# Kernel optimization log

Measured on AMD Instinct MI355X. Metric: run time of the kernel, lower is better.

Reference implementation:

```python
import jax, jax.numpy as jnp
import numpy as np

N = 50000      # nodes
E = 800000     # edges
F_IN = 128     # num_node_features
H = 128        # hidden_channels
C = 10         # num_classes
G = 512        # graphs in batch


def setup_inputs() -> dict:
    key = jax.random.key(0)
    ks = jax.random.split(key, 8)
    x = jax.random.normal(ks[0], (N, F_IN), dtype=jnp.float32)
    edge_index = jax.random.randint(ks[1], (2, E), 0, N, dtype=jnp.int64)
    batch = jnp.sort(jax.random.randint(ks[2], (N,), 0, G, dtype=jnp.int64))
    s = 1.0 / np.sqrt(F_IN)
    W1 = jax.random.normal(ks[3], (F_IN, H), dtype=jnp.float32) * s
    b1 = jnp.zeros((H,), dtype=jnp.float32)
    W2 = jax.random.normal(ks[4], (H, H), dtype=jnp.float32) * s
    b2 = jnp.zeros((H,), dtype=jnp.float32)
    Wl = jax.random.normal(ks[5], (H, C), dtype=jnp.float32) * s
    bl = jnp.zeros((C,), dtype=jnp.float32)
    return {"x": x, "edge_index": edge_index, "batch": batch,
            "W1": W1, "b1": b1, "W2": W2, "b2": b2, "Wl": Wl, "bl": bl}


def _gcn_conv(h, src, dst, deg_inv_sqrt, W, b):
    # PyG GCNConv: x @ W, then symmetric-normalized scatter-add with self-loops.
    h = h @ W                                   # [N, H]
    norm = deg_inv_sqrt[src] * deg_inv_sqrt[dst]  # [E]
    msg = h[src] * norm[:, None]                # gather + scale, [E, H]
    out = jax.ops.segment_sum(msg, dst, num_segments=N)
    # self-loop contribution (deg already includes +1):
    out = out + h * (deg_inv_sqrt * deg_inv_sqrt)[:, None]
    return out + b


def reference(x, edge_index, batch, W1, b1, W2, b2, Wl, bl):
    src, dst = edge_index[0], edge_index[1]
    # degree on destination nodes, +1 for self-loops (PyG default)
    deg = jax.ops.segment_sum(jnp.ones((E,), x.dtype), dst, num_segments=N) + 1.0
    deg_inv_sqrt = jax.lax.rsqrt(deg)

    h = jax.nn.relu(_gcn_conv(x, src, dst, deg_inv_sqrt, W1, b1))
    h = jax.nn.relu(_gcn_conv(h, src, dst, deg_inv_sqrt, W2, b2))

    # global mean pool over graphs
    sums = jax.ops.segment_sum(h, batch, num_segments=G)          # [G, H]
    counts = jax.ops.segment_sum(jnp.ones((N,), h.dtype), batch, num_segments=G)
    pooled = sums / jnp.clip(counts, 1.0)[:, None]
    # dropout p=0.5 is identity in eval mode
    return pooled @ Wl + bl
```

## Files before the change

kernel.cpp:

```cpp
#include <hip/hip_runtime.h>
#include <hip/hip_bf16.h>
#include <hip/hip_fp16.h>

typedef unsigned short ushort_t;
typedef unsigned int uint32;
typedef __attribute__((ext_vector_type(8))) short short8;
typedef __attribute__((ext_vector_type(4))) float floatx4;

#define KMAX 64
#define BSHIFT 6
#define BCAP2 1280
#define MAXBUK 800

__device__ __forceinline__ float bf2f(ushort_t u) {
    return __uint_as_float(((uint32)u) << 16);
}
__device__ __forceinline__ ushort_t f2bf(float f) {
    uint32 x = __float_as_uint(f);
    return (ushort_t)((x + 0x7fffu + ((x >> 16) & 1u)) >> 16);
}
__device__ __forceinline__ uint32 pack2h(float a, float b) {
    return (uint32)__half_as_ushort(__float2half(a)) |
           ((uint32)__half_as_ushort(__float2half(b)) << 16);
}
__device__ __forceinline__ float2 unpack2h(uint32 q) {
    __half2 hh = *reinterpret_cast<__half2*>(&q);
    return __half22float2(hh);
}
__device__ __forceinline__ float h16f(ushort_t u) {
    __half h = *reinterpret_cast<__half*>(&u);
    return __half2float(h);
}

__global__ __launch_bounds__(256) void bin_k(const int* __restrict__ ei,
                                             int* __restrict__ bcur,
                                             uint32* __restrict__ binned,
                                             int E, int nbuk) {
    __shared__ int hist[MAXBUK], lbase[MAXBUK];
    int tid = threadIdx.x;
    for (int i = tid; i < nbuk; i += 256) hist[i] = 0;
    __syncthreads();
    int base = blockIdx.x * 4096;
    uint32 ed[16];
    int bk[16], rk[16];
    #pragma unroll
    for (int i = 0; i < 16; ++i) {
        int e = base + i * 256 + tid;
        if (e < E) {
            int s = ei[e], d = ei[E + e];
            ed[i] = (uint32)s | ((uint32)d << 16);
            bk[i] = d >> BSHIFT;
            rk[i] = atomicAdd(&hist[bk[i]], 1);
        } else bk[i] = -1;
    }
    __syncthreads();
    for (int i = tid; i < nbuk; i += 256) lbase[i] = atomicAdd(&bcur[i], hist[i]);
    __syncthreads();
    #pragma unroll
    for (int i = 0; i < 16; ++i) {
        if (bk[i] >= 0) {
            int idx = lbase[bk[i]] + rk[i];
            if (idx < BCAP2) binned[(size_t)bk[i] * BCAP2 + idx] = ed[i];
        }
    }
}

__global__ __launch_bounds__(256) void fill4_k(const uint32* __restrict__ binned,
                                               const int* __restrict__ bcur,
                                               int* __restrict__ cnt,
                                               ushort_t* __restrict__ slot, int N) {
    __shared__ ushort_t ls[64 * KMAX];
    __shared__ int lc[64];
    int b = blockIdx.x;
    int tid = threadIdx.x;
    if (tid < 64) lc[tid] = 0;
    __syncthreads();
    int ne = bcur[b];
    if (ne > BCAP2) ne = BCAP2;
    const uint32* src = binned + (size_t)b * BCAP2;
    int nbase = b << BSHIFT;
    for (int i = tid; i < ne; i += 256) {
        uint32 ed = src[i];
        int s = (int)(ed & 0xFFFFu);
        int d = (int)(ed >> 16) - nbase;
        int p = atomicAdd(&lc[d], 1);
        if (p < KMAX) ls[(d << 6) + p] = (ushort_t)s;
    }
    __syncthreads();
    int nn = N - nbase;
    if (nn > 64) nn = 64;
    if (tid < 64 && tid < nn) cnt[nbase + tid] = lc[tid];
    uint4* gs = (uint4*)(slot + ((size_t)nbase << 6));
    const uint4* lsv = (const uint4*)ls;
    int totalv = nn * 8;
    for (int i = tid; i < totalv; i += 256) gs[i] = lsv[i];
}

__global__ __launch_bounds__(256) void gemm_k(const void* __restrict__ Av, int mode,
                                              const float* __restrict__ W,
                                              uint32* __restrict__ t2, int N,
                                              const int* __restrict__ cnt,
                                              const int* __restrict__ batch,
                                              int* __restrict__ gstart, int G,
                                              int do_bounds) {
    int tid = threadIdx.x;
    if (do_bounds) {
        int i = blockIdx.x * 256 + tid;
        if (i <= G) {
            int lo = 0, hi = N;
            while (lo < hi) {
                int mid = (lo + hi) >> 1;
                if (batch[mid] < i) lo = mid + 1; else hi = mid;
            }
            gstart[i] = lo;
        }
    }

    __shared__ ushort_t Wh[128][136];
    for (int i = tid; i < 128 * 128; i += 256) {
        int k = i >> 7, c = i & 127;
        Wh[c][k] = f2bf(W[i]);
    }
    __syncthreads();

    int wave = tid >> 6, lane = tid & 63;
    int row0 = blockIdx.x * 64 + wave * 16;
    int m = lane & 15;
    int arow = row0 + m;
    int koff = (lane >> 4) * 8;
    bool valid = arow < N;

    floatx4 acc[8];
    #pragma unroll
    for (int nt = 0; nt < 8; ++nt) acc[nt] = (floatx4){0.f, 0.f, 0.f, 0.f};

    for (int kk = 0; kk < 4; ++kk) {
        int k = kk * 32 + koff;
        short8 ah = (short8){0, 0, 0, 0, 0, 0, 0, 0};
        short8 al = (short8){0, 0, 0, 0, 0, 0, 0, 0};
        if (valid) {
            float v[8];
            if (mode == 0) {
                const float* p = (const float*)Av + (size_t)arow * 128 + k;
                floatx4 f0 = *(const floatx4*)p;
                floatx4 f1 = *(const floatx4*)(p + 4);
                v[0] = f0[0]; v[1] = f0[1]; v[2] = f0[2]; v[3] = f0[3];
                v[4] = f1[0]; v[5] = f1[1]; v[6] = f1[2]; v[7] = f1[3];
            } else {
                const uint32* hp = (const uint32*)Av + (size_t)arow * 64 + (k & 63);
                uint4 w0 = *(const uint4*)hp;
                uint4 w1 = *(const uint4*)(hp + 4);
                uint32 ws[8] = {w0.x, w0.y, w0.z, w0.w, w1.x, w1.y, w1.z, w1.w};
                bool hi = k >= 64;
                #pragma unroll
                for (int j = 0; j < 8; ++j) {
                    ushort_t u = hi ? (ushort_t)(ws[j] >> 16) : (ushort_t)(ws[j] & 0xFFFFu);
                    v[j] = fmaxf(h16f(u), 0.f);
                }
            }
            #pragma unroll
            for (int j = 0; j < 8; ++j) {
                ushort_t h = f2bf(v[j]);
                ah[j] = (short)h;
                al[j] = (short)f2bf(v[j] - bf2f(h));
            }
        }
        #pragma unroll
        for (int nt = 0; nt < 8; ++nt) {
            int col = nt * 16 + m;
            short8 bh = *(const short8*)(&Wh[col][k]);
            acc[nt] = __builtin_amdgcn_mfma_f32_16x16x32_bf16(ah, bh, acc[nt], 0, 0, 0);
            acc[nt] = __builtin_amdgcn_mfma_f32_16x16x32_bf16(al, bh, acc[nt], 0, 0, 0);
        }
    }

    int r0 = (lane >> 4) * 4;
    float dsc[4];
    #pragma unroll
    for (int r = 0; r < 4; ++r) {
        int row = row0 + r0 + r;
        dsc[r] = (row < N) ? rsqrtf((float)cnt[row] + 1.0f) : 0.f;
    }
    #pragma unroll
    for (int nt = 0; nt < 4; ++nt) {
        int c = nt * 16 + m;
        #pragma unroll
        for (int r = 0; r < 4; ++r) {
            int row = row0 + r0 + r;
            if (row < N)
                t2[(size_t)row * 64 + c] =
                    pack2h(acc[nt][r] * dsc[r], acc[nt + 4][r] * dsc[r]);
        }
    }
}

__global__ __launch_bounds__(256) void agg_k(const uint32* __restrict__ t2,
                                             const int* __restrict__ cnt,
                                             const ushort_t* __restrict__ slot,
                                             const float* __restrict__ bias,
                                             uint32* __restrict__ outp, int N) {
    int wave = threadIdx.x >> 6, lane = threadIdx.x & 63;
    int n = blockIdx.x * 4 + wave;
    if (n >= N) return;
    int deg = cnt[n];
    float d = rsqrtf((float)deg + 1.0f);
    if (deg > KMAX) deg = KMAX;
    float2 self = unpack2h(t2[(size_t)n * 64 + lane]);
    float acc0 = self.x;
    float acc1 = self.y;
    const ushort_t* sl = slot + (size_t)n * KMAX;
    int i = 0;
    for (; i + 16 <= deg; i += 16) {
        uint4 qa = *(const uint4*)(sl + i);
        uint4 qb = *(const uint4*)(sl + i + 8);
        uint32 sw[8] = {qa.x, qa.y, qa.z, qa.w, qb.x, qb.y, qb.z, qb.w};
        int s[16];
        #pragma unroll
        for (int u = 0; u < 8; ++u) {
            s[2 * u] = (int)(sw[u] & 0xFFFFu);
            s[2 * u + 1] = (int)(sw[u] >> 16);
        }
        float2 f[16];
        #pragma unroll
        for (int u = 0; u < 16; ++u)
            f[u] = unpack2h(t2[(size_t)s[u] * 64 + lane]);
        #pragma unroll
        for (int u = 0; u < 16; ++u) {
            acc0 += f[u].x;
            acc1 += f[u].y;
        }
    }
    for (; i + 4 <= deg; i += 4) {
        uint2 qa = *(const uint2*)(sl + i);
        int s[4] = {(int)(qa.x & 0xFFFFu), (int)(qa.x >> 16),
                    (int)(qa.y & 0xFFFFu), (int)(qa.y >> 16)};
        float2 f[4];
        #pragma unroll
        for (int u = 0; u < 4; ++u)
            f[u] = unpack2h(t2[(size_t)s[u] * 64 + lane]);
        #pragma unroll
        for (int u = 0; u < 4; ++u) {
            acc0 += f[u].x;
            acc1 += f[u].y;
        }
    }
    for (; i < deg; ++i) {
        float2 f = unpack2h(t2[(size_t)sl[i] * 64 + lane]);
        acc0 += f.x;
        acc1 += f.y;
    }
    acc0 = acc0 * d + bias[lane];
    acc1 = acc1 * d + bias[lane + 64];
    outp[(size_t)n * 64 + lane] = pack2h(acc0, acc1);
}

__global__ __launch_bounds__(256) void pool2_k(const uint32* __restrict__ h2,
                                               const int* __restrict__ gstart,
                                               const float* __restrict__ Wl,
                                               const float* __restrict__ bl,
                                               float* __restrict__ out, int C) {
    __shared__ float s0[256];
    __shared__ float s1[256];
    __shared__ float m[128];
    int g = blockIdx.x;
    int s = gstart[g], e = gstart[g + 1];
    int w = threadIdx.x & 63;
    int sub = threadIdx.x >> 6;
    float a0 = 0.f, a1 = 0.f;
    for (int n = s + sub; n < e; n += 4) {
        float2 f = unpack2h(h2[(size_t)n * 64 + w]);
        a0 += fmaxf(f.x, 0.f);
        a1 += fmaxf(f.y, 0.f);
    }
    s0[threadIdx.x] = a0;
    s1[threadIdx.x] = a1;
    __syncthreads();
    if (threadIdx.x < 64) {
        float inv = 1.f / fmaxf((float)(e - s), 1.f);
        m[w]      = (s0[w] + s0[w + 64] + s0[w + 128] + s0[w + 192]) * inv;
        m[w + 64] = (s1[w] + s1[w + 64] + s1[w + 128] + s1[w + 192]) * inv;
    }
    __syncthreads();
    if (threadIdx.x < C) {
        float sum = bl[threadIdx.x];
        #pragma unroll 4
        for (int jj = 0; jj < 128; ++jj)
            sum += m[jj] * Wl[jj * C + threadIdx.x];
        out[g * C + threadIdx.x] = sum;
    }
}

extern "C" void kernel_launch(void* const* d_in, const int* in_sizes, int n_in,
                              void* d_out, int out_size, void* d_ws, size_t ws_size,
                              hipStream_t stream) {
    const float* x   = (const float*)d_in[0];
    const int* ei    = (const int*)d_in[1];
    const int* batch = (const int*)d_in[2];
    const float* W1  = (const float*)d_in[3];
    const float* b1  = (const float*)d_in[4];
    const float* W2  = (const float*)d_in[5];
    const float* b2  = (const float*)d_in[6];
    const float* Wl  = (const float*)d_in[7];
    const float* bl  = (const float*)d_in[8];
    float* out = (float*)d_out;

    int N = in_sizes[2];
    int E = in_sizes[1] / 2;
    int C = in_sizes[8];
    int G = out_size / C;
    int nbuk = (N + 63) >> BSHIFT;

    char* w = (char*)d_ws;
    auto alloc = [&](size_t bytes) -> void* {
        void* p = (void*)w;
        w += (bytes + 255) & ~(size_t)255;
        return p;
    };
    int* bcur       = (int*)alloc((size_t)nbuk * 4);
    int* cnt        = (int*)alloc((size_t)N * 4);
    int* gstart     = (int*)alloc((size_t)(G + 1) * 4);
    ushort_t* slot  = (ushort_t*)alloc((size_t)nbuk * 64 * KMAX * 2);
    uint32* binned  = (uint32*)alloc((size_t)nbuk * BCAP2 * 4);
    uint32* t2      = (uint32*)alloc((size_t)N * 64 * 4);
    uint32* h1      = (uint32*)alloc((size_t)N * 64 * 4);
    uint32* h2      = (uint32*)alloc((size_t)N * 64 * 4);

    hipMemsetAsync(bcur, 0, (size_t)nbuk * 4, stream);

    int GB = (N + 63) / 64;
    int AB = (N + 3) / 4;
    int BB = (E + 4095) / 4096;

    bin_k<<<BB, 256, 0, stream>>>(ei, bcur, binned, E, nbuk);
    fill4_k<<<nbuk, 256, 0, stream>>>(binned, bcur, cnt, slot, N);
    gemm_k<<<GB, 256, 0, stream>>>((const void*)x, 0, W1, t2, N,
                                   cnt, batch, gstart, G, 1);
    agg_k<<<AB, 256, 0, stream>>>(t2, cnt, slot, b1, h1, N);
    gemm_k<<<GB, 256, 0, stream>>>((const void*)h1, 2, W2, t2, N,
                                   cnt, batch, gstart, G, 0);
    agg_k<<<AB, 256, 0, stream>>>(t2, cnt, slot, b2, h2, N);
    pool2_k<<<G, 256, 0, stream>>>(h2, gstart, Wl, bl, out, C);
}
```

Before: 222.8 us.

## Split aggregation feature columns across 4 grid phases with neighbor-parallel lanes

The aggregation kernel now launches four times as many blocks. Each phase handles a 16-word slice of the feature row, and the four lane groups in a wave each take a different neighbor, with results combined by cross-lane shuffles. The aim is more parallelism and more independent gathers in flight for low-degree nodes, in place of one wave walking the neighbor list serially. In exchange, each gather now touches 64-byte segments instead of full 256-byte rows, slot indices and per-node setup are read four times, masked lanes do wasted work, and a shuffle reduction is added.

```diff
diff --git a/kernel.cpp b/kernel.cpp
--- a/kernel.cpp
+++ b/kernel.cpp
@@ -198,60 +198,53 @@
                                              const int* __restrict__ cnt,
                                              const ushort_t* __restrict__ slot,
                                              const float* __restrict__ bias,
-                                             uint32* __restrict__ outp, int N) {
+                                             uint32* __restrict__ outp, int N, int AB) {
+    int phase = blockIdx.x / AB;
+    int blk = blockIdx.x - phase * AB;
     int wave = threadIdx.x >> 6, lane = threadIdx.x & 63;
-    int n = blockIdx.x * 4 + wave;
+    int n = blk * 4 + wave;
     if (n >= N) return;
+    int u = lane >> 4;
+    int l = lane & 15;
+    int w = phase * 16 + l;
+
     int deg = cnt[n];
     float d = rsqrtf((float)deg + 1.0f);
     if (deg > KMAX) deg = KMAX;
-    float2 self = unpack2h(t2[(size_t)n * 64 + lane]);
-    float acc0 = self.x;
-    float acc1 = self.y;
     const ushort_t* sl = slot + (size_t)n * KMAX;
-    int i = 0;
-    for (; i + 16 <= deg; i += 16) {
-        uint4 qa = *(const uint4*)(sl + i);
-        uint4 qb = *(const uint4*)(sl + i + 8);
-        uint32 sw[8] = {qa.x, qa.y, qa.z, qa.w, qb.x, qb.y, qb.z, qb.w};
-        int s[16];
-        #pragma unroll
-        for (int u = 0; u < 8; ++u) {
-            s[2 * u] = (int)(sw[u] & 0xFFFFu);
-            s[2 * u + 1] = (int)(sw[u] >> 16);
-        }
-        float2 f[16];
-        #pragma unroll
-        for (int u = 0; u < 16; ++u)
-            f[u] = unpack2h(t2[(size_t)s[u] * 64 + lane]);
-        #pragma unroll
-        for (int u = 0; u < 16; ++u) {
-            acc0 += f[u].x;
-            acc1 += f[u].y;
-        }
-    }
-    for (; i + 4 <= deg; i += 4) {
-        uint2 qa = *(const uint2*)(sl + i);
-        int s[4] = {(int)(qa.x & 0xFFFFu), (int)(qa.x >> 16),
-                    (int)(qa.y & 0xFFFFu), (int)(qa.y >> 16)};
-        float2 f[4];
-        #pragma unroll
-        for (int u = 0; u < 4; ++u)
-            f[u] = unpack2h(t2[(size_t)s[u] * 64 + lane]);
-        #pragma unroll
-        for (int u = 0; u < 4; ++u) {
-            acc0 += f[u].x;
-            acc1 += f[u].y;
-        }
-    }
-    for (; i < deg; ++i) {
-        float2 f = unpack2h(t2[(size_t)sl[i] * 64 + lane]);
-        acc0 += f.x;
-        acc1 += f.y;
-    }
-    acc0 = acc0 * d + bias[lane];
-    acc1 = acc1 * d + bias[lane + 64];
-    outp[(size_t)n * 64 + lane] = pack2h(acc0, acc1);
+
+    float2 self = unpack2h(t2[(size_t)n * 64 + w]);
+    float b0 = bias[w], b1 = bias[w + 64];
+
+    float a0 = 0.f, a1 = 0.f;
+    for (int i = 0; i < deg; i += 16) {
+        int si[4];
+        float mk[4];
+        #pragma unroll
+        for (int q = 0; q < 4; ++q) {
+            int idx = i + q * 4 + u;
+            bool v = idx < deg;
+            si[q] = v ? (int)sl[idx] : 0;
+            mk[q] = v ? 1.f : 0.f;
+        }
+        uint32 g[4];
+        #pragma unroll
+        for (int q = 0; q < 4; ++q)
+            g[q] = t2[(size_t)si[q] * 64 + w];
+        #pragma unroll
+        for (int q = 0; q < 4; ++q) {
+            float2 f = unpack2h(g[q]);
+            a0 += f.x * mk[q];
+            a1 += f.y * mk[q];
+        }
+    }
+    a0 += __shfl_xor(a0, 16); a1 += __shfl_xor(a1, 16);
+    a0 += __shfl_xor(a0, 32); a1 += __shfl_xor(a1, 32);
+    if (u == 0) {
+        float r0 = (a0 + self.x) * d + b0;
+        float r1 = (a1 + self.y) * d + b1;
+        outp[(size_t)n * 64 + w] = pack2h(r0, r1);
+    }
 }
 
 __global__ __launch_bounds__(256) void pool2_k(const uint32* __restrict__ h2,
@@ -335,9 +328,9 @@
     fill4_k<<<nbuk, 256, 0, stream>>>(binned, bcur, cnt, slot, N);
     gemm_k<<<GB, 256, 0, stream>>>((const void*)x, 0, W1, t2, N,
                                    cnt, batch, gstart, G, 1);
-    agg_k<<<AB, 256, 0, stream>>>(t2, cnt, slot, b1, h1, N);
+    agg_k<<<AB * 4, 256, 0, stream>>>(t2, cnt, slot, b1, h1, N, AB);
     gemm_k<<<GB, 256, 0, stream>>>((const void*)h1, 2, W2, t2, N,
                                    cnt, batch, gstart, G, 0);
-    agg_k<<<AB, 256, 0, stream>>>(t2, cnt, slot, b2, h2, N);
+    agg_k<<<AB * 4, 256, 0, stream>>>(t2, cnt, slot, b2, h2, N, AB);
     pool2_k<<<G, 256, 0, stream>>>(h2, gstart, Wl, bl, out, C);
 }
```

New measurement: 314.8 us. 1.41x slower.
